# Kernel optimization log

Measured on AMD Instinct MI355X. Metric: run time of the kernel, lower is better.

The kernel has to match this reference:

```python
import jax, jax.numpy as jnp
import numpy as np
import math

LENGTH_SEQUENSE = 300  # hardcoded scale in the original module (NOT d_k)


def setup_inputs() -> dict:
    key = jax.random.key(0)
    k1, k2 = jax.random.split(key)
    B, S, D_in, D_out = 256, 300, 512, 512
    x = jax.random.normal(k1, (B, S, D_in), dtype=jnp.float32)
    weight_matrix = jax.random.normal(k2, (3, D_in, D_out), dtype=jnp.float32) * 0.02
    return {"x": x, "weight_matrix": weight_matrix}


def reference(x, weight_matrix):
    # Q/K/V projections: [B,S,D_in] @ [D_in,D_out] -> [B,S,D_out]
    query = jnp.einsum('bsd,de->bse', x, weight_matrix[0])
    key_ = jnp.einsum('bsd,de->bse', x, weight_matrix[1])
    value = jnp.einsum('bsd,de->bse', x, weight_matrix[2])
    # scores: [B,S,S]; faithful to original: scaled by sqrt(length_sequense)=sqrt(300)
    scores = jnp.einsum('bqe,bke->bqk', query, key_) / math.sqrt(LENGTH_SEQUENSE)
    attn = jax.nn.softmax(scores, axis=-1)
    # output: [B,S,D_out]
    return jnp.einsum('bqk,bke->bqe', attn, value)
```

## Files before the change

### kernel.cpp

```cpp
#include <hip/hip_runtime.h>
#include <hip/hip_bf16.h>
#include <math.h>

typedef __attribute__((ext_vector_type(8))) __bf16 bf16x8;
typedef __attribute__((ext_vector_type(8))) short  s16x8;
typedef __attribute__((ext_vector_type(4))) float  f32x4;
union SB8 { s16x8 s; bf16x8 b; };

__device__ __forceinline__ unsigned short f2bf(float f) {
  unsigned int u = __builtin_bit_cast(unsigned int, f);
  u = u + 0x7FFFu + ((u >> 16) & 1u);
  return (unsigned short)(u >> 16);
}

__device__ __forceinline__ void glds16(const void* g, void* l) {
  __builtin_amdgcn_global_load_lds((const __attribute__((address_space(1))) void*)g,
                                   (__attribute__((address_space(3))) void*)l, 16, 0, 0);
}

#define B_  256
#define S_  300
#define D_  512
#define SP  320
#define M_  76800

__global__ __launch_bounds__(256) void k_cvt_x(const float* __restrict__ x,
                                               unsigned short* __restrict__ xb, int n8) {
  int i = blockIdx.x * blockDim.x + threadIdx.x;
  int stride = gridDim.x * blockDim.x;
  for (; i < n8; i += stride) {
    const float4* p = (const float4*)(x + (size_t)i * 8);
    float4 a = p[0], b = p[1];
    union { unsigned short u[8]; s16x8 v; } o;
    o.u[0]=f2bf(a.x); o.u[1]=f2bf(a.y); o.u[2]=f2bf(a.z); o.u[3]=f2bf(a.w);
    o.u[4]=f2bf(b.x); o.u[5]=f2bf(b.y); o.u[6]=f2bf(b.z); o.u[7]=f2bf(b.w);
    *(s16x8*)(xb + (size_t)i * 8) = o.v;
  }
}

__global__ __launch_bounds__(256) void k_wt(const float* __restrict__ w,
                                            unsigned short* __restrict__ wt) {
  int i = blockIdx.x * 256 + threadIdx.x;
  int p = i >> 18;
  int r = i & 262143;
  int k = r >> 9, n = r & 511;
  wt[p * 262144 + n * 512 + k] = f2bf(w[i]);
}

__global__ __launch_bounds__(256) void k_projQK(const unsigned short* __restrict__ xb,
                                                const unsigned short* __restrict__ wt,
                                                unsigned short* __restrict__ qkv) {
  __shared__ short As[2][128 * 64];
  __shared__ short Bs[2][128 * 64];
  int bid = blockIdx.x;
  int xc = bid & 7, j = bid >> 3;
  int mt = xc + 8 * (j >> 3);
  int tile = j & 7;
  int p  = tile >> 2;
  int n0 = (tile & 3) * 128;
  int rowBase = mt * 128;
  const unsigned short* wp = wt + p * 262144;
  unsigned short* outp = qkv + (size_t)p * ((size_t)M_ * 512);

  int tid = threadIdx.x, lane = tid & 63, wid = tid >> 6;
  int wr = wid >> 1, wc = wid & 1;
  int sr = lane >> 3;
  int ssg = ((lane & 7) ^ sr) * 8;
  int fr = lane & 15;
  int g  = lane >> 4;
  f32x4 acc[4][4] = {};

  for (int c = wid * 4; c < wid * 4 + 4; ++c) {
    glds16(xb + (size_t)(rowBase + c * 8 + sr) * 512 + ssg, &As[0][c * 512 + lane * 8]);
    glds16(wp + (size_t)(n0 + c * 8 + sr) * 512 + ssg, &Bs[0][c * 512 + lane * 8]);
  }
  __syncthreads();

  for (int t = 0; t < 8; ++t) {
    int cur = t & 1;
    if (t < 7) {
      int k0n = (t + 1) * 64;
      for (int c = wid * 4; c < wid * 4 + 4; ++c) {
        glds16(xb + (size_t)(rowBase + c * 8 + sr) * 512 + k0n + ssg,
               &As[cur ^ 1][c * 512 + lane * 8]);
        glds16(wp + (size_t)(n0 + c * 8 + sr) * 512 + k0n + ssg,
               &Bs[cur ^ 1][c * 512 + lane * 8]);
      }
    }
    SB8 aF[4][2], bF[4][2];
#pragma unroll
    for (int m = 0; m < 4; ++m) {
      int row = wr * 64 + m * 16 + fr;
#pragma unroll
      for (int kk = 0; kk < 2; ++kk) {
        int sl = ((kk << 2) + g) ^ (fr & 7);
        aF[m][kk].s = *(const s16x8*)&As[cur][row * 64 + sl * 8];
      }
    }
#pragma unroll
    for (int n = 0; n < 4; ++n) {
      int row = wc * 64 + n * 16 + fr;
#pragma unroll
      for (int kk = 0; kk < 2; ++kk) {
        int sl = ((kk << 2) + g) ^ (fr & 7);
        bF[n][kk].s = *(const s16x8*)&Bs[cur][row * 64 + sl * 8];
      }
    }
#pragma unroll
    for (int kk = 0; kk < 2; ++kk)
#pragma unroll
      for (int m = 0; m < 4; ++m)
#pragma unroll
        for (int n = 0; n < 4; ++n)
          acc[m][n] = __builtin_amdgcn_mfma_f32_16x16x32_bf16(aF[m][kk].b, bF[n][kk].b,
                                                              acc[m][n], 0, 0, 0);
    __syncthreads();
  }

  int fq = lane >> 4;
#pragma unroll
  for (int m = 0; m < 4; ++m)
#pragma unroll
    for (int n = 0; n < 4; ++n) {
      int row = rowBase + wr * 64 + m * 16 + fq * 4;
      int col = n0 + wc * 64 + n * 16 + fr;
      unsigned short* o = outp + (size_t)row * 512 + col;
#pragma unroll
      for (int jj = 0; jj < 4; ++jj)
        o[(size_t)jj * 512] = f2bf(acc[m][n][jj]);
    }
}

__global__ __launch_bounds__(256) void k_projV(const unsigned short* __restrict__ xb,
                                               const unsigned short* __restrict__ wt,
                                               unsigned short* __restrict__ vt) {
  __shared__ short As[2][128 * 64];
  __shared__ short Bs[2][128 * 64];
  int bid = blockIdx.x;
  int xc = bid & 7, j = bid >> 3;
  int mt = xc + 8 * (j >> 2);
  int n0 = (j & 3) * 128;
  int rowBase = mt * 128;
  const unsigned short* wp = wt + 2 * 262144;

  int tid = threadIdx.x, lane = tid & 63, wid = tid >> 6;
  int wr = wid >> 1, wc = wid & 1;
  int sr = lane >> 3;
  int ssg = ((lane & 7) ^ sr) * 8;
  int fr = lane & 15;
  int g  = lane >> 4;
  f32x4 acc[4][4] = {};

  for (int c = wid * 4; c < wid * 4 + 4; ++c) {
    glds16(xb + (size_t)(rowBase + c * 8 + sr) * 512 + ssg, &As[0][c * 512 + lane * 8]);
    glds16(wp + (size_t)(n0 + c * 8 + sr) * 512 + ssg, &Bs[0][c * 512 + lane * 8]);
  }
  __syncthreads();

  for (int t = 0; t < 8; ++t) {
    int cur = t & 1;
    if (t < 7) {
      int k0n = (t + 1) * 64;
      for (int c = wid * 4; c < wid * 4 + 4; ++c) {
        glds16(xb + (size_t)(rowBase + c * 8 + sr) * 512 + k0n + ssg,
               &As[cur ^ 1][c * 512 + lane * 8]);
        glds16(wp + (size_t)(n0 + c * 8 + sr) * 512 + k0n + ssg,
               &Bs[cur ^ 1][c * 512 + lane * 8]);
      }
    }
    SB8 aF[4][2], bF[4][2];
#pragma unroll
    for (int m = 0; m < 4; ++m) {
      int row = wr * 64 + m * 16 + fr;
#pragma unroll
      for (int kk = 0; kk < 2; ++kk) {
        int sl = ((kk << 2) + g) ^ (fr & 7);
        aF[m][kk].s = *(const s16x8*)&As[cur][row * 64 + sl * 8];
      }
    }
#pragma unroll
    for (int n = 0; n < 4; ++n) {
      int row = wc * 64 + n * 16 + fr;
#pragma unroll
      for (int kk = 0; kk < 2; ++kk) {
        int sl = ((kk << 2) + g) ^ (fr & 7);
        bF[n][kk].s = *(const s16x8*)&Bs[cur][row * 64 + sl * 8];
      }
    }
#pragma unroll
    for (int kk = 0; kk < 2; ++kk)
#pragma unroll
      for (int m = 0; m < 4; ++m)
#pragma unroll
        for (int n = 0; n < 4; ++n)
          acc[m][n] = __builtin_amdgcn_mfma_f32_16x16x32_bf16(aF[m][kk].b, bF[n][kk].b,
                                                              acc[m][n], 0, 0, 0);
    __syncthreads();
  }

  int fq = lane >> 4;
  short* T2 = &As[0][0];
#pragma unroll
  for (int m = 0; m < 4; ++m) {
    int s0 = wr * 64 + m * 16 + fq * 4;
#pragma unroll
    for (int n16 = 0; n16 < 4; ++n16) {
      int c = wc * 64 + n16 * 16 + fr;
      int idx = c * 128 + (s0 ^ ((c & 7) << 4));
      union { unsigned short u[4]; uint2 v; } w;
#pragma unroll
      for (int jj = 0; jj < 4; ++jj) w.u[jj] = f2bf(acc[m][n16][jj]);
      *(uint2*)&T2[idx] = w.v;
    }
  }
  __syncthreads();
  for (int i = 0; i < 8; ++i) {
    int u = i * 256 + tid;
    int n = u >> 4, ch = u & 15;
    int idx = n * 128 + ((ch * 8) ^ ((n & 7) << 4));
    s16x8 vv = *(const s16x8*)&T2[idx];
    size_t ncol = (size_t)(n0 + n);
#pragma unroll
    for (int h = 0; h < 2; ++h) {
      int gs = rowBase + ch * 8 + h * 4;
      int bb = (unsigned)gs / 300u;
      int sloc = gs - bb * 300;
      union { unsigned short u[4]; uint2 v; } w;
#pragma unroll
      for (int e = 0; e < 4; ++e) w.u[e] = (unsigned short)vv[h * 4 + e];
      *(uint2*)(vt + (size_t)bb * (512 * SP) + ncol * SP + sloc) = w.v;
    }
  }
}

__global__ __launch_bounds__(256) void k_attn_p(const unsigned short* __restrict__ Q,
                                                const unsigned short* __restrict__ K,
                                                unsigned short* __restrict__ P) {
  __shared__ union {
    struct { short q[32 * 512]; short k[2][320 * 32]; } s1;
    float S[32 * 321];
  } sm;
  __shared__ float invS[32];
  int bid = blockIdx.x;
  int xcd = bid & 7, slot = bid >> 3;
  int b = xcd * 32 + slot / 10;
  int qt = slot % 10;
  int qBase = qt * 32;
  const unsigned short* Qb = Q + (size_t)b * S_ * 512;
  const unsigned short* Kb = K + (size_t)b * S_ * 512;
  unsigned short* Pb = P + (size_t)b * S_ * SP;
  int tid = threadIdx.x, lane = tid & 63, wid = tid >> 6;
  int lr = lane >> 2;
  int sk = ((lane & 3) ^ (lr & 3)) * 8;
  int kg = (lane >> 4) * 8, fr = lane & 15;
  int g = lane >> 4;

  for (int c = wid * 8; c < wid * 8 + 8; ++c) {
    int qr = qBase + c; if (qr > 299) qr = 299;
    int ke = (lane * 8) ^ ((c & 7) * 8);
    glds16(Qb + (size_t)qr * 512 + ke, &sm.s1.q[c * 512 + lane * 8]);
  }
  for (int c = wid; c < 20; c += 4) {
    int kr = c * 16 + lr; if (kr > 299) kr = 299;
    glds16(Kb + (size_t)kr * 512 + sk, &sm.s1.k[0][c * 512 + lane * 8]);
  }
  __syncthreads();

  int ntBase = wid * 5;
  f32x4 acc[2][5] = {};

  for (int t = 0; t < 16; ++t) {
    int cur = t & 1;
    if (t < 15) {
      int k0n = (t + 1) * 32;
      for (int c = wid; c < 20; c += 4) {
        int kr = c * 16 + lr; if (kr > 299) kr = 299;
        glds16(Kb + (size_t)kr * 512 + k0n + sk, &sm.s1.k[cur ^ 1][c * 512 + lane * 8]);
      }
    }
    int k0 = t * 32;
    SB8 qF[2], kF[5];
#pragma unroll
    for (int m = 0; m < 2; ++m) {
      int r = m * 16 + fr;
      int ko = (k0 + kg) ^ ((r & 7) * 8);
      qF[m].s = *(const s16x8*)&sm.s1.q[r * 512 + ko];
    }
#pragma unroll
    for (int n = 0; n < 5; ++n) {
      int kslot = (g ^ (fr & 3)) * 8;
      kF[n].s = *(const s16x8*)&sm.s1.k[cur][((ntBase + n) * 16 + fr) * 32 + kslot];
    }
#pragma unroll
    for (int m = 0; m < 2; ++m)
#pragma unroll
      for (int n = 0; n < 5; ++n)
        acc[m][n] = __builtin_amdgcn_mfma_f32_16x16x32_bf16(qF[m].b, kF[n].b, acc[m][n], 0, 0, 0);
    __syncthreads();
  }

  const float scale = 0.05773502691896258f;
#pragma unroll
  for (int m = 0; m < 2; ++m)
#pragma unroll
    for (int n = 0; n < 5; ++n) {
      int col = (ntBase + n) * 16 + fr;
      int rb = m * 16 + (lane >> 4) * 4;
#pragma unroll
      for (int jj = 0; jj < 4; ++jj)
        sm.S[(rb + jj) * 321 + col] = acc[m][n][jj] * scale;
    }
  __syncthreads();

  {
    int r = tid >> 3, jj = tid & 7;
    int c0 = jj * 40;
    int cend = c0 + 40; if (cend > 300) cend = 300;
    const float* Sr = &sm.S[r * 321];
    float m0 = -1e30f, m1 = -1e30f, m2 = -1e30f, m3 = -1e30f;
    for (int c = c0; c < cend; c += 4) {
      m0 = fmaxf(m0, Sr[c]);     m1 = fmaxf(m1, Sr[c + 1]);
      m2 = fmaxf(m2, Sr[c + 2]); m3 = fmaxf(m3, Sr[c + 3]);
    }
    float mx = fmaxf(fmaxf(m0, m1), fmaxf(m2, m3));
    mx = fmaxf(mx, __shfl_xor(mx, 1));
    mx = fmaxf(mx, __shfl_xor(mx, 2));
    mx = fmaxf(mx, __shfl_xor(mx, 4));
    float s0 = 0.f, s1 = 0.f, s2 = 0.f, s3 = 0.f;
    float* Sw = &sm.S[r * 321];
    for (int c = c0; c < cend; c += 4) {
      float e0 = __expf(Sw[c] - mx);     Sw[c] = e0;     s0 += e0;
      float e1 = __expf(Sw[c + 1] - mx); Sw[c + 1] = e1; s1 += e1;
      float e2 = __expf(Sw[c + 2] - mx); Sw[c + 2] = e2; s2 += e2;
      float e3 = __expf(Sw[c + 3] - mx); Sw[c + 3] = e3; s3 += e3;
    }
    float sum = (s0 + s1) + (s2 + s3);
    sum += __shfl_xor(sum, 1);
    sum += __shfl_xor(sum, 2);
    sum += __shfl_xor(sum, 4);
    if (jj == 0) invS[r] = 1.0f / sum;
  }
  __syncthreads();

  {
    int r = tid >> 3, jj = tid & 7;
    int qrow = qBase + r;
    if (qrow < 300) {
      float inv = invS[r];
      int c0 = jj * 40;
      const float* Sr = &sm.S[r * 321];
#pragma unroll
      for (int i = 0; i < 5; ++i) {
        union { unsigned short u[8]; s16x8 v; } o;
#pragma unroll
        for (int j2 = 0; j2 < 8; ++j2) {
          int c = c0 + i * 8 + j2;
          o.u[j2] = (c < 300) ? f2bf(Sr[c] * inv) : (unsigned short)0;
        }
        *(s16x8*)(Pb + (size_t)qrow * SP + c0 + i * 8) = o.v;
      }
    }
  }
}

__global__ __launch_bounds__(256) void k_pv(const unsigned short* __restrict__ P,
                                            const unsigned short* __restrict__ Vt,
                                            float* __restrict__ O) {
  __shared__ short As[128 * 32];
  __shared__ short Bs[128 * 32];
  int bid = blockIdx.x;
  int xc = bid & 7, j = bid >> 3;
  int b = xc + 8 * (j / 12);
  int tile = j % 12;
  int mt = tile >> 2, n0 = (tile & 3) * 128;
  int rowBase = mt * 128;
  const unsigned short* Pb  = P  + (size_t)b * S_ * SP;
  const unsigned short* Vtb = Vt + (size_t)b * 512 * SP;
  float* Ob = O + (size_t)b * S_ * 512;
  int tid = threadIdx.x, lane = tid & 63, wid = tid >> 6;
  int wr = wid >> 1, wc = wid & 1;
  int sr4 = lane >> 2;
  int ss = ((lane & 3) ^ ((lane >> 3) & 3)) * 8;
  int fr = lane & 15;
  int g = lane >> 4;
  int sl = (g ^ ((fr >> 1) & 3)) * 8;
  f32x4 acc[4][4] = {};

  for (int t = 0; t < 10; ++t) {
    int k0 = t * 32;
    for (int c = wid * 2; c < wid * 2 + 2; ++c) {
      int row = rowBase + c * 16 + sr4; if (row > 299) row = 299;
      glds16(Pb + (size_t)row * SP + k0 + ss, &As[c * 512 + lane * 8]);
    }
    for (int c = wid * 2; c < wid * 2 + 2; ++c)
      glds16(Vtb + (size_t)(n0 + c * 16 + sr4) * SP + k0 + ss,
             &Bs[c * 512 + lane * 8]);
    __syncthreads();
    SB8 aF[4], bF[4];
#pragma unroll
    for (int m = 0; m < 4; ++m) {
      int row = wr * 64 + m * 16 + fr;
      aF[m].s = *(const s16x8*)&As[row * 32 + sl];
    }
#pragma unroll
    for (int n = 0; n < 4; ++n) {
      int row = wc * 64 + n * 16 + fr;
      bF[n].s = *(const s16x8*)&Bs[row * 32 + sl];
    }
#pragma unroll
    for (int m = 0; m < 4; ++m)
#pragma unroll
      for (int n = 0; n < 4; ++n)
        acc[m][n] = __builtin_amdgcn_mfma_f32_16x16x32_bf16(aF[m].b, bF[n].b, acc[m][n], 0, 0, 0);
    __syncthreads();
  }
  int fq = lane >> 4;
#pragma unroll
  for (int m = 0; m < 4; ++m)
#pragma unroll
    for (int n = 0; n < 4; ++n) {
      int col = n0 + wc * 64 + n * 16 + fr;
#pragma unroll
      for (int jj = 0; jj < 4; ++jj) {
        int row = rowBase + wr * 64 + m * 16 + fq * 4 + jj;
        if (row < 300) Ob[(size_t)row * 512 + col] = acc[m][n][jj];
      }
    }
}

extern "C" void kernel_launch(void* const* d_in, const int* in_sizes, int n_in,
                              void* d_out, int out_size, void* d_ws, size_t ws_size,
                              hipStream_t stream) {
  const float* x = (const float*)d_in[0];
  const float* w = (const float*)d_in[1];
  float* out = (float*)d_out;
  char* ws = (char*)d_ws;

  unsigned short* QK = (unsigned short*)d_out;
  unsigned short* Vt = (unsigned short*)(ws);
  unsigned short* xb = (unsigned short*)(ws + 83886080LL);
  unsigned short* Pp = xb;
  unsigned short* Wt = (unsigned short*)(ws + 162529280LL);

  k_cvt_x<<<2048, 256, 0, stream>>>(x, xb, 4915200);
  k_wt<<<3072, 256, 0, stream>>>(w, Wt);
  k_projQK<<<4800, 256, 0, stream>>>(xb, Wt, QK);
  k_projV<<<2400, 256, 0, stream>>>(xb, Wt, Vt);
  k_attn_p<<<2560, 256, 0, stream>>>(QK, QK + (size_t)M_ * 512, Pp);
  k_pv<<<3072, 256, 0, stream>>>(Pp, Vt, out);
}
```

Baseline: 423.2 us.

## Load Q fragments directly from global, shrink LDS, swizzle score buffer

In the attention-score kernel, Q fragments are now read straight from global memory (L1/L2) each k-step instead of being staged into a 32KB LDS tile. This cuts LDS use from roughly 72KB to about 41KB per block, which may allow more resident blocks per CU. The score buffer now uses an XOR swizzle with a 320 stride instead of 321 padding. The separate inverse-sum pass and its barrier are folded into the softmax pass. The cost is that Q global loads now sit inside the MFMA loop, which can add latency.

```diff
diff --git a/kernel.cpp b/kernel.cpp
--- a/kernel.cpp
+++ b/kernel.cpp
@@ -237,10 +237,9 @@
                                                 const unsigned short* __restrict__ K,
                                                 unsigned short* __restrict__ P) {
   __shared__ union {
-    struct { short q[32 * 512]; short k[2][320 * 32]; } s1;
-    float S[32 * 321];
+    short k[2][320 * 32];
+    float S[32 * 320];
   } sm;
-  __shared__ float invS[32];
   int bid = blockIdx.x;
   int xcd = bid & 7, slot = bid >> 3;
   int b = xcd * 32 + slot / 10;
@@ -255,14 +254,14 @@
   int kg = (lane >> 4) * 8, fr = lane & 15;
   int g = lane >> 4;
 
-  for (int c = wid * 8; c < wid * 8 + 8; ++c) {
-    int qr = qBase + c; if (qr > 299) qr = 299;
-    int ke = (lane * 8) ^ ((c & 7) * 8);
-    glds16(Qb + (size_t)qr * 512 + ke, &sm.s1.q[c * 512 + lane * 8]);
-  }
+  int qr0 = qBase + fr;      if (qr0 > 299) qr0 = 299;
+  int qr1 = qBase + 16 + fr; if (qr1 > 299) qr1 = 299;
+  const unsigned short* Qr0 = Qb + (size_t)qr0 * 512 + kg;
+  const unsigned short* Qr1 = Qb + (size_t)qr1 * 512 + kg;
+
   for (int c = wid; c < 20; c += 4) {
     int kr = c * 16 + lr; if (kr > 299) kr = 299;
-    glds16(Kb + (size_t)kr * 512 + sk, &sm.s1.k[0][c * 512 + lane * 8]);
+    glds16(Kb + (size_t)kr * 512 + sk, &sm.k[0][c * 512 + lane * 8]);
   }
   __syncthreads();
 
@@ -275,21 +274,17 @@
       int k0n = (t + 1) * 32;
       for (int c = wid; c < 20; c += 4) {
         int kr = c * 16 + lr; if (kr > 299) kr = 299;
-        glds16(Kb + (size_t)kr * 512 + k0n + sk, &sm.s1.k[cur ^ 1][c * 512 + lane * 8]);
+        glds16(Kb + (size_t)kr * 512 + k0n + sk, &sm.k[cur ^ 1][c * 512 + lane * 8]);
       }
     }
     int k0 = t * 32;
     SB8 qF[2], kF[5];
-#pragma unroll
-    for (int m = 0; m < 2; ++m) {
-      int r = m * 16 + fr;
-      int ko = (k0 + kg) ^ ((r & 7) * 8);
-      qF[m].s = *(const s16x8*)&sm.s1.q[r * 512 + ko];
-    }
+    qF[0].s = *(const s16x8*)(Qr0 + k0);
+    qF[1].s = *(const s16x8*)(Qr1 + k0);
 #pragma unroll
     for (int n = 0; n < 5; ++n) {
       int kslot = (g ^ (fr & 3)) * 8;
-      kF[n].s = *(const s16x8*)&sm.s1.k[cur][((ntBase + n) * 16 + fr) * 32 + kslot];
+      kF[n].s = *(const s16x8*)&sm.k[cur][((ntBase + n) * 16 + fr) * 32 + kslot];
     }
 #pragma unroll
     for (int m = 0; m < 2; ++m)
@@ -305,59 +300,55 @@
 #pragma unroll
     for (int n = 0; n < 5; ++n) {
       int col = (ntBase + n) * 16 + fr;
-      int rb = m * 16 + (lane >> 4) * 4;
+      int rb = m * 16 + g * 4;
 #pragma unroll
       for (int jj = 0; jj < 4; ++jj)
-        sm.S[(rb + jj) * 321 + col] = acc[m][n][jj] * scale;
+        sm.S[(rb + jj) * 320 + (col ^ (jj << 3))] = acc[m][n][jj] * scale;
     }
   __syncthreads();
 
   {
     int r = tid >> 3, jj = tid & 7;
+    int rx = (r & 3) << 3;
     int c0 = jj * 40;
     int cend = c0 + 40; if (cend > 300) cend = 300;
-    const float* Sr = &sm.S[r * 321];
+    float* Sr = &sm.S[r * 320];
     float m0 = -1e30f, m1 = -1e30f, m2 = -1e30f, m3 = -1e30f;
     for (int c = c0; c < cend; c += 4) {
-      m0 = fmaxf(m0, Sr[c]);     m1 = fmaxf(m1, Sr[c + 1]);
-      m2 = fmaxf(m2, Sr[c + 2]); m3 = fmaxf(m3, Sr[c + 3]);
+      int cs = c ^ rx;
+      m0 = fmaxf(m0, Sr[cs]);     m1 = fmaxf(m1, Sr[cs + 1]);
+      m2 = fmaxf(m2, Sr[cs + 2]); m3 = fmaxf(m3, Sr[cs + 3]);
     }
     float mx = fmaxf(fmaxf(m0, m1), fmaxf(m2, m3));
     mx = fmaxf(mx, __shfl_xor(mx, 1));
     mx = fmaxf(mx, __shfl_xor(mx, 2));
     mx = fmaxf(mx, __shfl_xor(mx, 4));
     float s0 = 0.f, s1 = 0.f, s2 = 0.f, s3 = 0.f;
-    float* Sw = &sm.S[r * 321];
     for (int c = c0; c < cend; c += 4) {
-      float e0 = __expf(Sw[c] - mx);     Sw[c] = e0;     s0 += e0;
-      float e1 = __expf(Sw[c + 1] - mx); Sw[c + 1] = e1; s1 += e1;
-      float e2 = __expf(Sw[c + 2] - mx); Sw[c + 2] = e2; s2 += e2;
-      float e3 = __expf(Sw[c + 3] - mx); Sw[c + 3] = e3; s3 += e3;
+      int cs = c ^ rx;
+      float e0 = __expf(Sr[cs] - mx);     Sr[cs] = e0;     s0 += e0;
+      float e1 = __expf(Sr[cs + 1] - mx); Sr[cs + 1] = e1; s1 += e1;
+      float e2 = __expf(Sr[cs + 2] - mx); Sr[cs + 2] = e2; s2 += e2;
+      float e3 = __expf(Sr[cs + 3] - mx); Sr[cs + 3] = e3; s3 += e3;
     }
     float sum = (s0 + s1) + (s2 + s3);
     sum += __shfl_xor(sum, 1);
     sum += __shfl_xor(sum, 2);
     sum += __shfl_xor(sum, 4);
-    if (jj == 0) invS[r] = 1.0f / sum;
-  }
-  __syncthreads();
-
-  {
-    int r = tid >> 3, jj = tid & 7;
+    float inv = 1.0f / sum;
     int qrow = qBase + r;
     if (qrow < 300) {
-      float inv = invS[r];
-      int c0 = jj * 40;
-      const float* Sr = &sm.S[r * 321];
 #pragma unroll
       for (int i = 0; i < 5; ++i) {
+        int cb = c0 + i * 8;
+        int cbs = cb ^ rx;
         union { unsigned short u[8]; s16x8 v; } o;
 #pragma unroll
-        for (int j2 = 0; j2 < 8; ++j2) {
-          int c = c0 + i * 8 + j2;
-          o.u[j2] = (c < 300) ? f2bf(Sr[c] * inv) : (unsigned short)0;
+        for (int e = 0; e < 8; ++e) {
+          int cc = cb + e;
+          o.u[e] = (cc < 300) ? f2bf(Sr[cbs + e] * inv) : (unsigned short)0;
         }
-        *(s16x8*)(Pb + (size_t)qrow * SP + c0 + i * 8) = o.v;
+        *(s16x8*)(Pb + (size_t)qrow * SP + cb) = o.v;
       }
     }
   }
```

After: 425.4 us. No clear change (+0.5%).
